# Kernel tuning notes

Measured on AMD Instinct MI355X. Metric: run time of the kernel, lower is better.

The kernel has to match this reference:

```python
import jax, jax.numpy as jnp
import numpy as np

B, T, V, H = 32, 512, 32000, 1024


def setup_inputs() -> dict:
    key = jax.random.key(0)
    k0, k1, k2, k3 = jax.random.split(key, 4)
    x = jax.random.randint(k0, (B, T), 0, V, dtype=jnp.int32)
    hidden = jnp.zeros((B, H), jnp.float32)
    embedding = jax.random.normal(k1, (V, H), jnp.float32) * 0.02
    # glorot-ish scaling for the gate kernels
    kernel = jax.random.normal(k2, (H, 3 * H), jnp.float32) * (1.0 / np.sqrt(H))
    recurrent_kernel = jax.random.normal(k3, (H, 3 * H), jnp.float32) * (1.0 / np.sqrt(H))
    bias = jnp.zeros((2, 3 * H), jnp.float32)  # [input_bias, recurrent_bias] (reset_after=True)
    return {"x": x, "hidden": hidden, "embedding": embedding,
            "kernel": kernel, "recurrent_kernel": recurrent_kernel, "bias": bias}


def reference(x, hidden, embedding, kernel, recurrent_kernel, bias):
    mask = (x != 0)                      # mask_zero=True: token id 0 is padding
    emb = embedding[x]                   # [B, T, H]
    b_i, b_r = bias[0], bias[1]

    def step(h, inp):
        x_t, m_t = inp                   # x_t: [B, H], m_t: [B]
        gx = x_t @ kernel + b_i          # [B, 3H]
        gh = h @ recurrent_kernel + b_r  # [B, 3H] (reset_after=True)
        xz, xr, xn = jnp.split(gx, 3, axis=-1)
        hz, hr, hn = jnp.split(gh, 3, axis=-1)
        z = jax.nn.sigmoid(xz + hz)
        r = jax.nn.sigmoid(xr + hr)
        hh = jnp.tanh(xn + r * hn)
        h_new = z * h + (1.0 - z) * hh
        # masked steps: carry previous state/output forward
        h_new = jnp.where(m_t[:, None], h_new, h)
        return h_new, h_new

    xs = (jnp.swapaxes(emb, 0, 1), jnp.swapaxes(mask, 0, 1))  # time-major
    state, outs = jax.lax.scan(step, hidden, xs)
    output = jnp.swapaxes(outs, 0, 1)    # [B, T, H]
    return output, state
```

## Files before the change

### kernel.cpp

```cpp
#include <hip/hip_runtime.h>
#include <hip/hip_bf16.h>
#include <math.h>


#define B_  32
#define T_  512
#define H_  1024
#define H3  3072
#define NG  64
#define UPG 16

typedef short short8 __attribute__((ext_vector_type(8)));
typedef float float4_ __attribute__((ext_vector_type(4)));
typedef int   int4_  __attribute__((ext_vector_type(4)));
typedef unsigned short u16;
typedef unsigned int u32;

__device__ __forceinline__ float bf2f(u16 u) {
  union { unsigned i; float f; } v; v.i = ((unsigned)u) << 16; return v.f;
}
__device__ __forceinline__ u16 f2bf(float f) {
  union { float f; unsigned i; } v; v.f = f;
  unsigned r = v.i + 0x7FFFu + ((v.i >> 16) & 1u);
  return (u16)(r >> 16);
}
__device__ __forceinline__ float ldf(const void* p, size_t i, int f32) {
  return f32 ? ((const float*)p)[i] : bf2f(((const u16*)p)[i]);
}
__device__ __forceinline__ short8 ld8(const void* base, size_t off, int f32) {
  short8 r;
  if (f32) {
    const float* p = (const float*)base + off;
    float4_ a = *(const float4_*)p;
    float4_ b = *(const float4_*)(p + 4);
    r[0]=(short)f2bf(a[0]); r[1]=(short)f2bf(a[1]); r[2]=(short)f2bf(a[2]); r[3]=(short)f2bf(a[3]);
    r[4]=(short)f2bf(b[0]); r[5]=(short)f2bf(b[1]); r[6]=(short)f2bf(b[2]); r[7]=(short)f2bf(b[3]);
  } else {
    r = *(const short8*)((const u16*)base + off);
  }
  return r;
}

__device__ __forceinline__ u32 aload32(const u32* p) {
  return __hip_atomic_load((u32*)p, __ATOMIC_RELAXED, __HIP_MEMORY_SCOPE_AGENT);
}
__device__ __forceinline__ void astore32(u32* p, u32 v) {
  __hip_atomic_store(p, v, __ATOMIC_RELAXED, __HIP_MEMORY_SCOPE_AGENT);
}
__device__ __forceinline__ u32 pack2(float h0, float h1) {
  return ((u32)f2bf(h1) << 16) | (u32)f2bf(h0);
}

__global__ __launch_bounds__(256) void detect_norm(
    const void* __restrict__ emb, const void* __restrict__ bias,
    int* dflag, float* __restrict__ bias_c, u32* __restrict__ ep) {
  __shared__ int cnt;
  __shared__ int sflag;
  if (threadIdx.x == 0) cnt = 0;
  __syncthreads();
  const unsigned* e = (const unsigned*)emb;
  const unsigned lo = e[threadIdx.x] & 0xFFFFu;
  if (((lo >> 7) & 0xFFu) >= 128u) atomicAdd(&cnt, 1);
  __syncthreads();
  if (threadIdx.x == 0) {
    sflag = (cnt > 32) ? 1 : 0;
    *dflag = sflag;
  }
  __syncthreads();
  const int f32 = sflag;
  for (int i = threadIdx.x; i < 2 * H3; i += 256) bias_c[i] = ldf(bias, i, f32);
  astore32(&ep[threadIdx.x], 0u);
  astore32(&ep[threadIdx.x + 256], 0u);
}

__global__ __launch_bounds__(256) void transpose_kernel(
    const void* __restrict__ W, const void* __restrict__ R,
    u16* __restrict__ Wt, u16* __restrict__ Rt, const int* dflag) {
  __shared__ u16 tile[32][33];
  const int f32 = *dflag;
  const void* src = blockIdx.z ? R : W;
  u16* dst = blockIdx.z ? Rt : Wt;
  int k0 = blockIdx.x * 32, n0 = blockIdx.y * 32;
  int c = threadIdx.x & 31, r8 = threadIdx.x >> 5;
  for (int rr = r8; rr < 32; rr += 8)
    tile[rr][c] = f2bf(ldf(src, (size_t)(k0 + rr) * H3 + n0 + c, f32));
  __syncthreads();
  for (int rr = r8; rr < 32; rr += 8)
    dst[(size_t)(n0 + rr) * H_ + k0 + c] = tile[c][rr];
}

__global__ __launch_bounds__(256) void gx_gemm(
    const int* __restrict__ x, const void* __restrict__ emb,
    const u16* __restrict__ Wt, const float* __restrict__ bias_c,
    u16* __restrict__ gx, const int* dflag) {
  __shared__ u16 Al[128][72];
  __shared__ u16 Bl[128][72];
  __shared__ int tok[128];
  const int f32 = *dflag;
  const int tid = threadIdx.x;
  const int n0 = blockIdx.x * 128;
  const int t0 = blockIdx.y * 4;
  if (tid < 128) { int b = tid >> 2, dt = tid & 3; tok[tid] = x[b * T_ + t0 + dt]; }
  __syncthreads();
  const int lane = tid & 63, w = tid >> 6;
  const int l = lane & 15, q = lane >> 4;
  const int wm = w >> 1, wn = w & 1;
  float4_ acc[4][4];
  for (int i = 0; i < 4; i++) for (int j = 0; j < 4; j++) acc[i][j] = (float4_)0.0f;
  const int row = tid >> 1, half = tid & 1;
  for (int k0 = 0; k0 < H_; k0 += 64) {
    const size_t offA = (size_t)tok[row] * H_ + k0 + half * 32;
    const u16* srcB = Wt + (size_t)(n0 + row) * H_ + k0 + half * 32;
#pragma unroll
    for (int c = 0; c < 4; c++) {
      *(short8*)&Al[row][half * 32 + c * 8] = ld8(emb, offA + c * 8, f32);
      *(short8*)&Bl[row][half * 32 + c * 8] = *(const short8*)(srcB + c * 8);
    }
    __syncthreads();
#pragma unroll
    for (int ks = 0; ks < 2; ks++) {
      const int kk = ks * 32 + q * 8;
      short8 af[4], bfv[4];
#pragma unroll
      for (int mi = 0; mi < 4; mi++) af[mi] = *(const short8*)&Al[wm * 64 + mi * 16 + l][kk];
#pragma unroll
      for (int ni = 0; ni < 4; ni++) bfv[ni] = *(const short8*)&Bl[wn * 64 + ni * 16 + l][kk];
#pragma unroll
      for (int mi = 0; mi < 4; mi++)
#pragma unroll
        for (int ni = 0; ni < 4; ni++)
          acc[mi][ni] = __builtin_amdgcn_mfma_f32_16x16x32_bf16(af[mi], bfv[ni], acc[mi][ni], 0, 0, 0);
    }
    __syncthreads();
  }
  for (int ni = 0; ni < 4; ni++) {
    const int n = n0 + wn * 64 + ni * 16 + l;
    const float bi = bias_c[n];
    for (int mi = 0; mi < 4; mi++) {
#pragma unroll
      for (int rr = 0; rr < 4; rr++) {
        const int rloc = wm * 64 + mi * 16 + q * 4 + rr;
        const int b = rloc >> 2, dt = rloc & 3;
        gx[((size_t)(t0 + dt) * H3 + n) * B_ + b] = f2bf(acc[mi][ni][rr] + bi);
      }
    }
  }
}

__global__ __launch_bounds__(256, 1) void gru_recur(
    const int* __restrict__ x, const void* __restrict__ hidden,
    const u16* __restrict__ Rt, const float* __restrict__ bias_c,
    const u16* __restrict__ gx, u32* __restrict__ hdat,
    u32* __restrict__ ep, void* __restrict__ out, const int* dflag) {
  extern __shared__ char smem[];
  u16* Rl = (u16*)smem;
  float* P = (float*)(smem + 99072);
  unsigned* mw = (unsigned*)(smem + 99072 + 51200);
  const int f32o = *dflag;
  const int g = blockIdx.x, tid = threadIdx.x;
  const int lane = tid & 63, w = tid >> 6;
  const int l = lane & 15, q = lane >> 4;
  float* outf = (float*)out;
  u16* outb = (u16*)out;

  for (int i = tid; i < 48 * 128; i += 256) {
    const int cc = i >> 7, ch = i & 127;
    const int c = cc >> 4, u = cc & 15;
    *(short8*)&Rl[cc * 1032 + ch * 8] =
        *(const short8*)(Rt + (size_t)(c * H_ + g * UPG + u) * H_ + ch * 8);
  }
  for (int i = tid; i < 512; i += 256) mw[i] = 0u;
  __syncthreads();
  for (int i = tid; i < B_ * T_; i += 256) {
    const int b = i >> 9, t = i & 511;
    if (x[i] != 0) atomicOr(&mw[t], 1u << b);
  }

  const int b = tid & 31, up = tid >> 5;
  const int col0 = g * UPG + 2 * up;
  float br[2][3], hp[2];
#pragma unroll
  for (int p = 0; p < 2; p++) {
    const int col = col0 + p;
    br[p][0] = bias_c[H3 + col];
    br[p][1] = bias_c[H3 + H_ + col];
    br[p][2] = bias_c[H3 + 2 * H_ + col];
    hp[p] = ldf(hidden, (size_t)b * H_ + col, f32o);
  }
  astore32(&hdat[16384 + (size_t)(g * 8 + up) * 32 + b], pack2(hp[0], hp[1]));
  __builtin_amdgcn_s_waitcnt(0);
  __builtin_amdgcn_sched_barrier(0);
  if ((tid & 63) == 0) astore32(&ep[256 + g * 4 + w], 1u);
  __syncthreads();

  for (int t = 0; t < T_; t++) {
    float gxv[2][3];
#pragma unroll
    for (int p = 0; p < 2; p++) {
      const int col = col0 + p;
#pragma unroll
      for (int c = 0; c < 3; c++)
        gxv[p][c] = bf2f(gx[((size_t)t * H3 + c * H_ + col) * B_ + b]);
    }

    const u32 aw = (u32)(t + 1);
    const u32* epp = ep + (size_t)((t + 1) & 1) * 256;
    const int lid = lane;
    while (1) {
      u32 e0 = aload32(epp + lid);
      u32 e1 = aload32(epp + lid + 64);
      u32 e2 = aload32(epp + lid + 128);
      u32 e3 = aload32(epp + lid + 192);
      if (__all(e0 == aw && e1 == aw && e2 == aw && e3 == aw)) break;
      __builtin_amdgcn_s_sleep(1);
    }
    __builtin_amdgcn_sched_barrier(0);

    const u32* hd = hdat + (size_t)((t + 1) & 1) * 16384;
    const int jb0 = w * 128 + q * 4;
    u32 va[8][8];
#pragma unroll
    for (int kk = 0; kk < 8; kk++) {
      const u32* p = hd + (size_t)(jb0 + kk * 16) * 32 + l;
#pragma unroll
      for (int i = 0; i < 4; i++) {
        va[kk][i]     = aload32(p + i * 32);
        va[kk][4 + i] = aload32(p + i * 32 + 16);
      }
    }

    float4_ acc[2][3];
#pragma unroll
    for (int mt = 0; mt < 2; mt++)
#pragma unroll
      for (int nt = 0; nt < 3; nt++) acc[mt][nt] = (float4_)0.0f;
#pragma unroll
    for (int kk = 0; kk < 8; kk++) {
      const int k = w * 256 + kk * 32 + q * 8;
      union { int4_ d; short8 s; } ua, ub;
#pragma unroll
      for (int i = 0; i < 4; i++) {
        ua.d[i] = (int)va[kk][i];
        ub.d[i] = (int)va[kk][4 + i];
      }
      const short8 a0 = ua.s, a1 = ub.s;
      const short8 r0 = *(const short8*)&Rl[(0 * 16 + l) * 1032 + k];
      const short8 r1 = *(const short8*)&Rl[(1 * 16 + l) * 1032 + k];
      const short8 r2 = *(const short8*)&Rl[(2 * 16 + l) * 1032 + k];
      acc[0][0] = __builtin_amdgcn_mfma_f32_16x16x32_bf16(a0, r0, acc[0][0], 0, 0, 0);
      acc[0][1] = __builtin_amdgcn_mfma_f32_16x16x32_bf16(a0, r1, acc[0][1], 0, 0, 0);
      acc[0][2] = __builtin_amdgcn_mfma_f32_16x16x32_bf16(a0, r2, acc[0][2], 0, 0, 0);
      acc[1][0] = __builtin_amdgcn_mfma_f32_16x16x32_bf16(a1, r0, acc[1][0], 0, 0, 0);
      acc[1][1] = __builtin_amdgcn_mfma_f32_16x16x32_bf16(a1, r1, acc[1][1], 0, 0, 0);
      acc[1][2] = __builtin_amdgcn_mfma_f32_16x16x32_bf16(a1, r2, acc[1][2], 0, 0, 0);
    }
    float* Pc = P + (t & 1) * 6400;
#pragma unroll
    for (int mt = 0; mt < 2; mt++)
#pragma unroll
      for (int nt = 0; nt < 3; nt++)
#pragma unroll
        for (int rr = 0; rr < 4; rr++)
          Pc[w * 1600 + (mt * 16 + q * 4 + rr) * 50 + nt * 16 + l] = acc[mt][nt][rr];
    __syncthreads();

    const unsigned mword = mw[t];
#pragma unroll
    for (int p = 0; p < 2; p++) {
      const int u = 2 * up + p;
      float hz = 0.f, hr = 0.f, hn = 0.f;
#pragma unroll
      for (int ww = 0; ww < 4; ww++) {
        const float* Pb = Pc + ww * 1600 + b * 50;
        hz += Pb[u]; hr += Pb[16 + u]; hn += Pb[32 + u];
      }
      hz += br[p][0]; hr += br[p][1]; hn += br[p][2];
      const float z = 1.f / (1.f + __expf(-(gxv[p][0] + hz)));
      const float r = 1.f / (1.f + __expf(-(gxv[p][1] + hr)));
      float nn = gxv[p][2] + r * hn;
      nn = fminf(fmaxf(nn, -15.f), 15.f);
      const float e2 = __expf(2.f * nn);
      const float th = (e2 - 1.f) / (e2 + 1.f);
      float hnew = z * hp[p] + (1.f - z) * th;
      if (!((mword >> b) & 1u)) hnew = hp[p];
      hp[p] = hnew;
    }
    astore32(&hdat[(size_t)(t & 1) * 16384 + (size_t)(g * 8 + up) * 32 + b],
             pack2(hp[0], hp[1]));
    __builtin_amdgcn_s_waitcnt(0);
    __builtin_amdgcn_sched_barrier(0);
    if ((tid & 63) == 0) astore32(&ep[(size_t)(t & 1) * 256 + g * 4 + w], (u32)(t + 2));
    const size_t oi = ((size_t)b * T_ + t) * H_ + col0;
    if (f32o) {
      __builtin_nontemporal_store(hp[0], outf + oi);
      __builtin_nontemporal_store(hp[1], outf + oi + 1);
    } else {
      const unsigned pw = ((unsigned)f2bf(hp[1]) << 16) | (unsigned)f2bf(hp[0]);
      __builtin_nontemporal_store(pw, (unsigned*)(outb + oi));
    }
  }
  {
    const size_t oi = (size_t)B_ * T_ * H_ + (size_t)b * H_ + col0;
    if (f32o) {
      __builtin_nontemporal_store(hp[0], outf + oi);
      __builtin_nontemporal_store(hp[1], outf + oi + 1);
    } else {
      const unsigned pw = ((unsigned)f2bf(hp[1]) << 16) | (unsigned)f2bf(hp[0]);
      __builtin_nontemporal_store(pw, (unsigned*)(outb + oi));
    }
  }
}

extern "C" void kernel_launch(void* const* d_in, const int* in_sizes, int n_in,
                              void* d_out, int out_size, void* d_ws, size_t ws_size,
                              hipStream_t stream) {
  const int* x       = (const int*)d_in[0];
  const void* hidden = d_in[1];
  const void* emb    = d_in[2];
  const void* W      = d_in[3];
  const void* R      = d_in[4];
  const void* bias   = d_in[5];
  char* ws = (char*)d_ws;
  u16*   gx      = (u16*)ws;
  u16*   Wt      = (u16*)(ws + 100663296);
  u16*   Rt      = (u16*)(ws + 106954752);
  u32*   hdat    = (u32*)(ws + 113246208);
  u32*   ep      = (u32*)(ws + 113246208 + 131072);
  int*   dflag   = (int*)(ws + 113508352);
  float* bias_c  = (float*)(ws + 113508608);

  hipLaunchKernelGGL(detect_norm, dim3(1), dim3(256), 0, stream,
                     emb, bias, dflag, bias_c, ep);
  hipLaunchKernelGGL(transpose_kernel, dim3(32, 96, 2), dim3(256), 0, stream,
                     W, R, Wt, Rt, dflag);
  hipLaunchKernelGGL(gx_gemm, dim3(24, 128), dim3(256), 0, stream,
                     x, emb, Wt, bias_c, gx, dflag);
  hipFuncSetAttribute((const void*)gru_recur, hipFuncAttributeMaxDynamicSharedMemorySize, 152320);
  hipLaunchKernelGGL(gru_recur, dim3(NG), dim3(256), 152320, stream,
                     x, hidden, Rt, bias_c, gx, hdat, ep, d_out, dflag);
}
```

Measured before the change: 2.735 ms.

## Repack hidden-state exchange buffer for 64-bit loads and per-wave flag polling

```diff
diff --git a/kernel.cpp b/kernel.cpp
--- a/kernel.cpp
+++ b/kernel.cpp
@@ -12,9 +12,9 @@
 
 typedef short short8 __attribute__((ext_vector_type(8)));
 typedef float float4_ __attribute__((ext_vector_type(4)));
-typedef int   int4_  __attribute__((ext_vector_type(4)));
 typedef unsigned short u16;
 typedef unsigned int u32;
+typedef unsigned long long ull;
 
 __device__ __forceinline__ float bf2f(u16 u) {
   union { unsigned i; float f; } v; v.i = ((unsigned)u) << 16; return v.f;
@@ -45,6 +45,12 @@
   return __hip_atomic_load((u32*)p, __ATOMIC_RELAXED, __HIP_MEMORY_SCOPE_AGENT);
 }
 __device__ __forceinline__ void astore32(u32* p, u32 v) {
+  __hip_atomic_store(p, v, __ATOMIC_RELAXED, __HIP_MEMORY_SCOPE_AGENT);
+}
+__device__ __forceinline__ ull aload64(const ull* p) {
+  return __hip_atomic_load((ull*)p, __ATOMIC_RELAXED, __HIP_MEMORY_SCOPE_AGENT);
+}
+__device__ __forceinline__ void astore64(ull* p, ull v) {
   __hip_atomic_store(p, v, __ATOMIC_RELAXED, __HIP_MEMORY_SCOPE_AGENT);
 }
 __device__ __forceinline__ u32 pack2(float h0, float h1) {
@@ -150,7 +156,7 @@
 __global__ __launch_bounds__(256, 1) void gru_recur(
     const int* __restrict__ x, const void* __restrict__ hidden,
     const u16* __restrict__ Rt, const float* __restrict__ bias_c,
-    const u16* __restrict__ gx, u32* __restrict__ hdat,
+    const u16* __restrict__ gx, ull* __restrict__ hdat64,
     u32* __restrict__ ep, void* __restrict__ out, const int* dflag) {
   extern __shared__ char smem[];
   u16* Rl = (u16*)smem;
@@ -187,10 +193,15 @@
     br[p][2] = bias_c[H3 + 2 * H_ + col];
     hp[p] = ldf(hidden, (size_t)b * H_ + col, f32o);
   }
-  astore32(&hdat[16384 + (size_t)(g * 8 + up) * 32 + b], pack2(hp[0], hp[1]));
+  {
+    const u32 pk = pack2(hp[0], hp[1]);
+    const u32 npk = (u32)__shfl_down((int)pk, 32);
+    if (lane < 32)
+      astore64(&hdat64[8192 + (size_t)b * 256 + g * 4 + w], (ull)pk | ((ull)npk << 32));
+  }
   __builtin_amdgcn_s_waitcnt(0);
   __builtin_amdgcn_sched_barrier(0);
-  if ((tid & 63) == 0) astore32(&ep[256 + g * 4 + w], 1u);
+  if (lane == 0) astore32(&ep[256 + g * 4 + w], 1u);
   __syncthreads();
 
   for (int t = 0; t < T_; t++) {
@@ -204,29 +215,24 @@
     }
 
     const u32 aw = (u32)(t + 1);
-    const u32* epp = ep + (size_t)((t + 1) & 1) * 256;
-    const int lid = lane;
+    const u32* epp = ep + (size_t)((t + 1) & 1) * 256 + w * 64;
     while (1) {
-      u32 e0 = aload32(epp + lid);
-      u32 e1 = aload32(epp + lid + 64);
-      u32 e2 = aload32(epp + lid + 128);
-      u32 e3 = aload32(epp + lid + 192);
-      if (__all(e0 == aw && e1 == aw && e2 == aw && e3 == aw)) break;
+      u32 e = aload32(epp + lane);
+      if (__all(e == aw)) break;
       __builtin_amdgcn_s_sleep(1);
     }
     __builtin_amdgcn_sched_barrier(0);
 
-    const u32* hd = hdat + (size_t)((t + 1) & 1) * 16384;
-    const int jb0 = w * 128 + q * 4;
-    u32 va[8][8];
+    const ull* hd = hdat64 + (size_t)((t + 1) & 1) * 8192;
+    const int cbase = w * 64 + q * 2;
+    ull va64[8][4];
 #pragma unroll
     for (int kk = 0; kk < 8; kk++) {
-      const u32* p = hd + (size_t)(jb0 + kk * 16) * 32 + l;
-#pragma unroll
-      for (int i = 0; i < 4; i++) {
-        va[kk][i]     = aload32(p + i * 32);
-        va[kk][4 + i] = aload32(p + i * 32 + 16);
-      }
+      const ull* p0 = hd + (size_t)l * 256 + cbase + 8 * kk;
+      va64[kk][0] = aload64(p0);
+      va64[kk][1] = aload64(p0 + 1);
+      va64[kk][2] = aload64(p0 + 4096);
+      va64[kk][3] = aload64(p0 + 4097);
     }
 
     float4_ acc[2][3];
@@ -237,12 +243,9 @@
 #pragma unroll
     for (int kk = 0; kk < 8; kk++) {
       const int k = w * 256 + kk * 32 + q * 8;
-      union { int4_ d; short8 s; } ua, ub;
-#pragma unroll
-      for (int i = 0; i < 4; i++) {
-        ua.d[i] = (int)va[kk][i];
-        ub.d[i] = (int)va[kk][4 + i];
-      }
+      union { ull d[2]; short8 s; } ua, ub;
+      ua.d[0] = va64[kk][0]; ua.d[1] = va64[kk][1];
+      ub.d[0] = va64[kk][2]; ub.d[1] = va64[kk][3];
       const short8 a0 = ua.s, a1 = ub.s;
       const short8 r0 = *(const short8*)&Rl[(0 * 16 + l) * 1032 + k];
       const short8 r1 = *(const short8*)&Rl[(1 * 16 + l) * 1032 + k];
@@ -285,11 +288,16 @@
       if (!((mword >> b) & 1u)) hnew = hp[p];
       hp[p] = hnew;
     }
-    astore32(&hdat[(size_t)(t & 1) * 16384 + (size_t)(g * 8 + up) * 32 + b],
-             pack2(hp[0], hp[1]));
+    {
+      const u32 pk = pack2(hp[0], hp[1]);
+      const u32 npk = (u32)__shfl_down((int)pk, 32);
+      if (lane < 32)
+        astore64(&hdat64[(size_t)(t & 1) * 8192 + (size_t)b * 256 + g * 4 + w],
+                 (ull)pk | ((ull)npk << 32));
+    }
     __builtin_amdgcn_s_waitcnt(0);
     __builtin_amdgcn_sched_barrier(0);
-    if ((tid & 63) == 0) astore32(&ep[(size_t)(t & 1) * 256 + g * 4 + w], (u32)(t + 2));
+    if (lane == 0) astore32(&ep[(size_t)(t & 1) * 256 + g * 4 + w], (u32)(t + 2));
     const size_t oi = ((size_t)b * T_ + t) * H_ + col0;
     if (f32o) {
       __builtin_nontemporal_store(hp[0], outf + oi);
@@ -324,7 +332,7 @@
   u16*   gx      = (u16*)ws;
   u16*   Wt      = (u16*)(ws + 100663296);
   u16*   Rt      = (u16*)(ws + 106954752);
-  u32*   hdat    = (u32*)(ws + 113246208);
+  ull*   hdat64  = (ull*)(ws + 113246208);
   u32*   ep      = (u32*)(ws + 113246208 + 131072);
   int*   dflag   = (int*)(ws + 113508352);
   float* bias_c  = (float*)(ws + 113508608);
@@ -337,5 +345,5 @@
                      x, emb, Wt, bias_c, gx, dflag);
   hipFuncSetAttribute((const void*)gru_recur, hipFuncAttributeMaxDynamicSharedMemorySize, 152320);
   hipLaunchKernelGGL(gru_recur, dim3(NG), dim3(256), 152320, stream,
-                     x, hidden, Rt, bias_c, gx, hdat, ep, d_out, dflag);
-}
+                     x, hidden, Rt, bias_c, gx, hdat64, ep, d_out, dflag);
+}
```

Result: slower. 4.194 ms (+53.4%).

## Consume hidden-state chunks as producers signal readiness instead of global barrier

Applied to the files above, without the earlier changes.

```diff
diff --git a/kernel.cpp b/kernel.cpp
--- a/kernel.cpp
+++ b/kernel.cpp
@@ -15,6 +15,7 @@
 typedef int   int4_  __attribute__((ext_vector_type(4)));
 typedef unsigned short u16;
 typedef unsigned int u32;
+typedef unsigned long long ull;
 
 __device__ __forceinline__ float bf2f(u16 u) {
   union { unsigned i; float f; } v; v.i = ((unsigned)u) << 16; return v.f;
@@ -155,7 +156,7 @@
   extern __shared__ char smem[];
   u16* Rl = (u16*)smem;
   float* P = (float*)(smem + 99072);
-  unsigned* mw = (unsigned*)(smem + 99072 + 51200);
+  unsigned* mw = (unsigned*)(smem + 99072 + 50176);
   const int f32o = *dflag;
   const int g = blockIdx.x, tid = threadIdx.x;
   const int lane = tid & 63, w = tid >> 6;
@@ -190,7 +191,7 @@
   astore32(&hdat[16384 + (size_t)(g * 8 + up) * 32 + b], pack2(hp[0], hp[1]));
   __builtin_amdgcn_s_waitcnt(0);
   __builtin_amdgcn_sched_barrier(0);
-  if ((tid & 63) == 0) astore32(&ep[256 + g * 4 + w], 1u);
+  if (lane == 0) astore32(&ep[256 + g * 4 + w], 1u);
   __syncthreads();
 
   for (int t = 0; t < T_; t++) {
@@ -204,64 +205,66 @@
     }
 
     const u32 aw = (u32)(t + 1);
-    const u32* epp = ep + (size_t)((t + 1) & 1) * 256;
-    const int lid = lane;
-    while (1) {
-      u32 e0 = aload32(epp + lid);
-      u32 e1 = aload32(epp + lid + 64);
-      u32 e2 = aload32(epp + lid + 128);
-      u32 e3 = aload32(epp + lid + 192);
-      if (__all(e0 == aw && e1 == aw && e2 == aw && e3 == aw)) break;
-      __builtin_amdgcn_s_sleep(1);
-    }
-    __builtin_amdgcn_sched_barrier(0);
-
+    const u32* epp = ep + (size_t)((t + 1) & 1) * 256 + w * 64;
     const u32* hd = hdat + (size_t)((t + 1) & 1) * 16384;
     const int jb0 = w * 128 + q * 4;
+    float4_ acc[2][3];
+#pragma unroll
+    for (int mt = 0; mt < 2; mt++)
+#pragma unroll
+      for (int nt = 0; nt < 3; nt++) acc[mt][nt] = (float4_)0.0f;
+
+    u32 done = 0;
     u32 va[8][8];
-#pragma unroll
-    for (int kk = 0; kk < 8; kk++) {
-      const u32* p = hd + (size_t)(jb0 + kk * 16) * 32 + l;
-#pragma unroll
-      for (int i = 0; i < 4; i++) {
-        va[kk][i]     = aload32(p + i * 32);
-        va[kk][4 + i] = aload32(p + i * 32 + 16);
+    while (done != 0xFFu) {
+      const u32 e = aload32(epp + lane);
+      const ull rdy = __ballot(e == aw);
+      u32 newly = 0;
+#pragma unroll
+      for (int kk = 0; kk < 8; kk++)
+        if (!(done & (1u << kk)) && ((u32)(rdy >> (kk * 8)) & 0xFFu) == 0xFFu)
+          newly |= 1u << kk;
+#pragma unroll
+      for (int kk = 0; kk < 8; kk++) if (newly & (1u << kk)) {
+        const u32* p = hd + (size_t)(jb0 + kk * 16) * 32 + l;
+#pragma unroll
+        for (int i = 0; i < 4; i++) {
+          va[kk][i]     = aload32(p + i * 32);
+          va[kk][4 + i] = aload32(p + i * 32 + 16);
+        }
       }
-    }
-
-    float4_ acc[2][3];
+#pragma unroll
+      for (int kk = 0; kk < 8; kk++) if (newly & (1u << kk)) {
+        const int k = w * 256 + kk * 32 + q * 8;
+        union { int4_ d; short8 s; } ua, ub;
+#pragma unroll
+        for (int i = 0; i < 4; i++) {
+          ua.d[i] = (int)va[kk][i];
+          ub.d[i] = (int)va[kk][4 + i];
+        }
+        const short8 a0 = ua.s, a1 = ub.s;
+        const short8 r0 = *(const short8*)&Rl[(0 * 16 + l) * 1032 + k];
+        const short8 r1 = *(const short8*)&Rl[(1 * 16 + l) * 1032 + k];
+        const short8 r2 = *(const short8*)&Rl[(2 * 16 + l) * 1032 + k];
+        acc[0][0] = __builtin_amdgcn_mfma_f32_16x16x32_bf16(a0, r0, acc[0][0], 0, 0, 0);
+        acc[0][1] = __builtin_amdgcn_mfma_f32_16x16x32_bf16(a0, r1, acc[0][1], 0, 0, 0);
+        acc[0][2] = __builtin_amdgcn_mfma_f32_16x16x32_bf16(a0, r2, acc[0][2], 0, 0, 0);
+        acc[1][0] = __builtin_amdgcn_mfma_f32_16x16x32_bf16(a1, r0, acc[1][0], 0, 0, 0);
+        acc[1][1] = __builtin_amdgcn_mfma_f32_16x16x32_bf16(a1, r1, acc[1][1], 0, 0, 0);
+        acc[1][2] = __builtin_amdgcn_mfma_f32_16x16x32_bf16(a1, r2, acc[1][2], 0, 0, 0);
+      }
+      done |= newly;
+      if (done != 0xFFu) __builtin_amdgcn_s_sleep(1);
+    }
+
+    float* Pc = P + (t & 1) * 6272;
 #pragma unroll
     for (int mt = 0; mt < 2; mt++)
 #pragma unroll
-      for (int nt = 0; nt < 3; nt++) acc[mt][nt] = (float4_)0.0f;
-#pragma unroll
-    for (int kk = 0; kk < 8; kk++) {
-      const int k = w * 256 + kk * 32 + q * 8;
-      union { int4_ d; short8 s; } ua, ub;
-#pragma unroll
-      for (int i = 0; i < 4; i++) {
-        ua.d[i] = (int)va[kk][i];
-        ub.d[i] = (int)va[kk][4 + i];
-      }
-      const short8 a0 = ua.s, a1 = ub.s;
-      const short8 r0 = *(const short8*)&Rl[(0 * 16 + l) * 1032 + k];
-      const short8 r1 = *(const short8*)&Rl[(1 * 16 + l) * 1032 + k];
-      const short8 r2 = *(const short8*)&Rl[(2 * 16 + l) * 1032 + k];
-      acc[0][0] = __builtin_amdgcn_mfma_f32_16x16x32_bf16(a0, r0, acc[0][0], 0, 0, 0);
-      acc[0][1] = __builtin_amdgcn_mfma_f32_16x16x32_bf16(a0, r1, acc[0][1], 0, 0, 0);
-      acc[0][2] = __builtin_amdgcn_mfma_f32_16x16x32_bf16(a0, r2, acc[0][2], 0, 0, 0);
-      acc[1][0] = __builtin_amdgcn_mfma_f32_16x16x32_bf16(a1, r0, acc[1][0], 0, 0, 0);
-      acc[1][1] = __builtin_amdgcn_mfma_f32_16x16x32_bf16(a1, r1, acc[1][1], 0, 0, 0);
-      acc[1][2] = __builtin_amdgcn_mfma_f32_16x16x32_bf16(a1, r2, acc[1][2], 0, 0, 0);
-    }
-    float* Pc = P + (t & 1) * 6400;
-#pragma unroll
-    for (int mt = 0; mt < 2; mt++)
-#pragma unroll
       for (int nt = 0; nt < 3; nt++)
 #pragma unroll
         for (int rr = 0; rr < 4; rr++)
-          Pc[w * 1600 + (mt * 16 + q * 4 + rr) * 50 + nt * 16 + l] = acc[mt][nt][rr];
+          Pc[w * 1568 + (mt * 16 + q * 4 + rr) * 49 + nt * 16 + l] = acc[mt][nt][rr];
     __syncthreads();
 
     const unsigned mword = mw[t];
@@ -271,7 +274,7 @@
       float hz = 0.f, hr = 0.f, hn = 0.f;
 #pragma unroll
       for (int ww = 0; ww < 4; ww++) {
-        const float* Pb = Pc + ww * 1600 + b * 50;
+        const float* Pb = Pc + ww * 1568 + b * 49;
         hz += Pb[u]; hr += Pb[16 + u]; hn += Pb[32 + u];
       }
       hz += br[p][0]; hr += br[p][1]; hn += br[p][2];
@@ -289,7 +292,7 @@
              pack2(hp[0], hp[1]));
     __builtin_amdgcn_s_waitcnt(0);
     __builtin_amdgcn_sched_barrier(0);
-    if ((tid & 63) == 0) astore32(&ep[(size_t)(t & 1) * 256 + g * 4 + w], (u32)(t + 2));
+    if (lane == 0) astore32(&ep[(size_t)(t & 1) * 256 + g * 4 + w], (u32)(t + 2));
     const size_t oi = ((size_t)b * T_ + t) * H_ + col0;
     if (f32o) {
       __builtin_nontemporal_store(hp[0], outf + oi);
@@ -335,7 +338,7 @@
                      W, R, Wt, Rt, dflag);
   hipLaunchKernelGGL(gx_gemm, dim3(24, 128), dim3(256), 0, stream,
                      x, emb, Wt, bias_c, gx, dflag);
-  hipFuncSetAttribute((const void*)gru_recur, hipFuncAttributeMaxDynamicSharedMemorySize, 152320);
-  hipLaunchKernelGGL(gru_recur, dim3(NG), dim3(256), 152320, stream,
+  hipFuncSetAttribute((const void*)gru_recur, hipFuncAttributeMaxDynamicSharedMemorySize, 151296);
+  hipLaunchKernelGGL(gru_recur, dim3(NG), dim3(256), 151296, stream,
                      x, hidden, Rt, bias_c, gx, hdat, ep, d_out, dflag);
 }
```

Result: slower. 2.837 ms (+3.8%).
